# Kernel tuning notes

Hardware: AMD Instinct MI355X
Metric: run time of the kernel (lower is better)

## Reference

```python
import jax, jax.numpy as jnp
import numpy as np

BITS = 4            # OPU.bits
VEC = 64            # OPU.input_vector_len / weight_vector_len
QMAX = 2 ** (BITS - 1) - 1   # 7


def ste_round(x):
    # straight-through round (onn_round)
    return x + jax.lax.stop_gradient(jnp.round(x) - x)


@jax.custom_vjp
def onn_dot_sum(x, w):
    # x: [N, R, VEC], w: [VEC, R, M]
    # per-chunk matmul -> clamp to int8 range -> binarize (>=0 -> 1) -> sum over chunks
    s = jnp.einsum('nrc,crm->nrm', x, w)
    s = jnp.clip(s, -128.0, 127.0)
    return jnp.where(s < 0, 0.0, 1.0).sum(axis=1)  # [N, M]


def _onn_dot_fwd(x, w):
    return onn_dot_sum(x, w), (x, w)


def _onn_dot_bwd(res, g):
    # onn_dot_fun.backward: straight-through past clamp+threshold;
    # each chunk receives the same grad g (sum over chunks).
    x, w = res
    gx = jnp.einsum('nm,crm->nrc', g, w)
    gw = jnp.einsum('nrc,nm->crm', x, g)
    return gx, gw


onn_dot_sum.defvjp(_onn_dot_fwd, _onn_dot_bwd)


def _onn_conv2d(inp, weight):
    B, C, H, W = inp.shape
    Cout, Cin, k, _ = weight.shape
    pad = (k - 1) // 2  # SAME, stride=1
    # im2col (matches torch F.unfold channel-major ordering: C, kh, kw)
    xp = jnp.pad(inp, ((0, 0), (0, 0), (pad, pad), (pad, pad)))
    patches = jnp.stack([xp[:, :, i:i + H, j:j + W]
                         for i in range(k) for j in range(k)], axis=2)  # [B,C,k*k,H,W]
    inp_unf = patches.reshape(B, C * k * k, H * W).transpose(0, 2, 1)    # [B,L,D]
    # weight quantization: STE round + clamp to 4-bit signed range
    scale = (2 ** BITS - 1) / (weight.max() - weight.min() + 1e-9)
    wq = jnp.clip(ste_round(weight * scale), -QMAX, QMAX)
    w_ = wq.reshape(Cout, -1).T                                          # [D, Cout]
    D = C * k * k
    repeats = -(-D // VEC)
    padD = VEC * repeats - D
    x = jnp.pad(inp_unf, ((0, 0), (0, 0), (0, padD))).reshape(B * H * W, repeats, VEC)
    wpad = jnp.pad(w_, ((0, padD), (0, 0)))                              # [VEC*R, Cout]
    wr = wpad.T.reshape(Cout, repeats, VEC).transpose(2, 1, 0)           # [VEC,R,Cout]
    temp = onn_dot_sum(x, wr)                                            # [B*L, Cout]
    return temp.reshape(B, H * W, Cout).transpose(0, 2, 1).reshape(B, Cout, H, W)


def setup_inputs() -> dict:
    key = jax.random.key(0)
    k1, k2 = jax.random.split(key)
    B, Cin, H, W = 16, 128, 32, 32
    Cout, k = 256, 3
    inp = jax.random.normal(k1, (B, Cin, H, W), dtype=jnp.float32)
    fan_in = Cin * k * k
    bound = 1.0 / np.sqrt(fan_in)  # kaiming_uniform with a=sqrt(5)
    weight = jax.random.uniform(k2, (Cout, Cin, k, k), dtype=jnp.float32,
                                minval=-bound, maxval=bound)
    return {"inp": inp, "weight": weight}


def reference(inp, weight):
    return _onn_conv2d(inp, weight)
```

## Files before the change

kernel.cpp:

```cpp
#include <hip/hip_runtime.h>


#define TAU 0.03f
#define HITCAP 2048

typedef short short8 __attribute__((ext_vector_type(8)));
typedef float f32x4 __attribute__((ext_vector_type(4)));
typedef unsigned int uv4 __attribute__((ext_vector_type(4)));

__device__ __forceinline__ unsigned short bf16rn(float v) {
    unsigned u = __float_as_uint(v);
    unsigned r = u + 0x7fffu + ((u >> 16) & 1u);
    return (unsigned short)(r >> 16);
}

__global__ __launch_bounds__(256) void k_prep(const float* __restrict__ w,
                                              const float* __restrict__ inp,
                                              float* __restrict__ pmin,
                                              float* __restrict__ pmax,
                                              unsigned* __restrict__ xpk) {
    if (blockIdx.x < 64) {
        int tid = blockIdx.x * 256 + threadIdx.x;
        float vmin = 1e30f, vmax = -1e30f;
        for (int i = tid; i < 294912; i += 64 * 256) {
            float v = w[i];
            vmin = fminf(vmin, v);
            vmax = fmaxf(vmax, v);
        }
        #pragma unroll
        for (int off = 32; off > 0; off >>= 1) {
            vmin = fminf(vmin, __shfl_down(vmin, off, 64));
            vmax = fmaxf(vmax, __shfl_down(vmax, off, 64));
        }
        __shared__ float smin[4], smax[4];
        int wave = threadIdx.x >> 6;
        if ((threadIdx.x & 63) == 0) { smin[wave] = vmin; smax[wave] = vmax; }
        __syncthreads();
        if (threadIdx.x == 0) {
            #pragma unroll
            for (int i = 1; i < 4; i++) {
                vmin = fminf(vmin, smin[i]);
                vmax = fmaxf(vmax, smax[i]);
            }
            pmin[blockIdx.x] = vmin;
            pmax[blockIdx.x] = vmax;
        }
    } else {
        int bc = blockIdx.x - 64;
        const float* src = inp + (size_t)bc * 1024;
        unsigned* dst = xpk + (size_t)bc * 1156;
        #pragma unroll
        for (int i = 0; i < 5; ++i) {
            int idx = threadIdx.x + i * 256;
            if (idx < 1156) {
                int yy = idx / 34, xx = idx - yy * 34;
                float v = 0.0f;
                int ys = yy - 1, xs_ = xx - 1;
                if ((unsigned)ys < 32u && (unsigned)xs_ < 32u) v = src[ys * 32 + xs_];
                unsigned short h = bf16rn(v);
                float hf = __uint_as_float((unsigned)h << 16);
                unsigned short l = bf16rn(v - hf);
                dst[idx] = (unsigned)h | ((unsigned)l << 16);
            }
        }
    }
}

__device__ __forceinline__ float block_scale(const float* pmin, const float* pmax,
                                             float* sca_lds) {
    int t = threadIdx.x;
    if (t < 64) {
        float vmin = pmin[t];
        float vmax = pmax[t];
        #pragma unroll
        for (int off = 32; off > 0; off >>= 1) {
            vmin = fminf(vmin, __shfl_down(vmin, off, 64));
            vmax = fmaxf(vmax, __shfl_down(vmax, off, 64));
        }
        if (t == 0) {
            float tt = __fadd_rn(__fsub_rn(vmax, vmin), 1e-9f);
            *sca_lds = __fdiv_rn(15.0f, tt);
        }
    }
    __syncthreads();
    return *sca_lds;
}

__global__ __launch_bounds__(256) void k_quantb(const float* __restrict__ w,
                                                const float* __restrict__ pmin,
                                                const float* __restrict__ pmax,
                                                uv4* __restrict__ wqb) {
    __shared__ float sca;
    float s = block_scale(pmin, pmax, &sca);
    int slot = blockIdx.x * 256 + threadIdx.x;
    int lane = slot & 63;
    int sub = slot >> 6;
    int khalf = sub & 1;
    int mt = (sub >> 1) & 3;
    int gr = sub >> 3;
    int g = gr / 18, r = gr - g * 18;
    int m = g * 64 + mt * 16 + (lane & 15);
    int dbase = r * 64 + khalf * 32 + (lane >> 4) * 8;
    const float* wp = w + (size_t)m * 1152 + dbase;
    unsigned o[4];
    #pragma unroll
    for (int p = 0; p < 4; ++p) {
        float q0 = rintf(__fmul_rn(wp[2 * p], s));
        float q1 = rintf(__fmul_rn(wp[2 * p + 1], s));
        q0 = fminf(fmaxf(q0, -7.0f), 7.0f);
        q1 = fminf(fmaxf(q1, -7.0f), 7.0f);
        o[p] = (unsigned)bf16rn(q0) | ((unsigned)bf16rn(q1) << 16);
    }
    uv4 v; v.x = o[0]; v.y = o[1]; v.z = o[2]; v.w = o[3];
    wqb[slot] = v;
}

#define XLD(o) (*reinterpret_cast<const unsigned*>(xwB + (o)))

#define ISSUE_B(rr, dst) do {                                                  \
    const int4* _oa = reinterpret_cast<const int4*>(&ofs_s[(rr) * 64 + quad * 8]); \
    int4 _o0 = _oa[0], _o1 = _oa[1];                                           \
    const int4* _ob = reinterpret_cast<const int4*>(&ofs_s[(rr) * 64 + 32 + quad * 8]); \
    int4 _o2 = _ob[0], _o3 = _ob[1];                                           \
    dst[0] = XLD(_o0.x); dst[1] = XLD(_o0.y); dst[2] = XLD(_o0.z); dst[3] = XLD(_o0.w); \
    dst[4] = XLD(_o1.x); dst[5] = XLD(_o1.y); dst[6] = XLD(_o1.z); dst[7] = XLD(_o1.w); \
    dst[8] = XLD(_o2.x); dst[9] = XLD(_o2.y); dst[10] = XLD(_o2.z); dst[11] = XLD(_o2.w); \
    dst[12] = XLD(_o3.x); dst[13] = XLD(_o3.y); dst[14] = XLD(_o3.z); dst[15] = XLD(_o3.w); \
} while (0)

__global__ __launch_bounds__(256) void k_main(const unsigned* __restrict__ xpk,
                                              const uv4* __restrict__ wqb,
                                              const float* __restrict__ inp,
                                              const float* __restrict__ weight,
                                              const float* __restrict__ pmin,
                                              const float* __restrict__ pmax,
                                              float* __restrict__ out) {
    __shared__ alignas(16) int ofs_s[1152];
    __shared__ unsigned hitbuf[HITCAP];
    __shared__ unsigned hitcnt;
    __shared__ float sca;

    const int t = threadIdx.x;
    if (t == 0) hitcnt = 0u;
    float sc = block_scale(pmin, pmax, &sca);
    for (int k = t; k < 1152; k += 256) {
        int cin = k / 9;
        int rem = k - cin * 9;
        int kh = rem / 3;
        int kw = rem - kh * 3;
        ofs_s[k] = (cin * 1156 + kh * 34 + kw) * 4;
    }
    __syncthreads();

    const int lane = t & 63;
    const int wv = t >> 6;
    const int quad = lane >> 4;
    const int nl = lane & 15;
    const int n0 = blockIdx.x * 64;
    const int g = blockIdx.y;
    const int b = n0 >> 10;

    const int sy_w = ((n0 & 1023) >> 5) + (wv >> 1);
    const int col0 = (wv & 1) * 16;
    const unsigned* __restrict__ xw =
        xpk + (size_t)b * (128 * 1156) + sy_w * 34 + col0 + nl;
    const char* __restrict__ xwB = (const char*)xw;
    const uv4* __restrict__ aw = wqb + (size_t)g * (18 * 512) + lane;

    int counts[4][4] = {};

    unsigned pb[16];
    ISSUE_B(0, pb);
    short8 ac0 = __builtin_bit_cast(short8, aw[0]);
    short8 ac1 = __builtin_bit_cast(short8, aw[64]);

    for (int r = 0; r < 18; ++r) {
        short8 bhi[2], blo[2];
        #pragma unroll
        for (int kh2 = 0; kh2 < 2; ++kh2) {
            union { unsigned d[4]; short8 v; } H, L;
            #pragma unroll
            for (int p = 0; p < 4; ++p) {
                unsigned ua = pb[kh2 * 8 + 2 * p], ub = pb[kh2 * 8 + 2 * p + 1];
                H.d[p] = __builtin_amdgcn_perm(ub, ua, 0x05040100u);
                L.d[p] = __builtin_amdgcn_perm(ub, ua, 0x07060302u);
            }
            bhi[kh2] = H.v;
            blo[kh2] = L.v;
        }

        const int rn = (r < 17) ? r + 1 : 17;
        ISSUE_B(rn, pb);

        f32x4 accs[4];
        unsigned hm = 0u;
        #pragma unroll
        for (int mt = 0; mt < 4; ++mt) {
            const int pn = (mt == 3) ? rn * 512 : (r * 512 + (mt + 1) * 128);
            short8 an0 = __builtin_bit_cast(short8, aw[pn]);
            short8 an1 = __builtin_bit_cast(short8, aw[pn + 64]);

            f32x4 acc = {0.0f, 0.0f, 0.0f, 0.0f};
            acc = __builtin_amdgcn_mfma_f32_16x16x32_bf16(ac0, bhi[0], acc, 0, 0, 0);
            acc = __builtin_amdgcn_mfma_f32_16x16x32_bf16(ac1, bhi[1], acc, 0, 0, 0);
            acc = __builtin_amdgcn_mfma_f32_16x16x32_bf16(ac0, blo[0], acc, 0, 0, 0);
            acc = __builtin_amdgcn_mfma_f32_16x16x32_bf16(ac1, blo[1], acc, 0, 0, 0);
            accs[mt] = acc;
            #pragma unroll
            for (int i = 0; i < 4; ++i) {
                float s = acc[i];
                counts[mt][i] += (s >= 0.0f) ? 1 : 0;
                hm |= (__builtin_fabsf(s) < TAU ? 1u : 0u) << (mt * 4 + i);
            }
            ac0 = an0;
            ac1 = an1;
        }

        if (__any((int)hm)) {
            #pragma unroll
            for (int mt = 0; mt < 4; ++mt)
                #pragma unroll
                for (int i = 0; i < 4; ++i)
                    if (hm & (1u << (mt * 4 + i))) {
                        float s = accs[mt][i];
                        int ge = (s >= 0.0f) ? 1 : 0;
                        unsigned idx = atomicAdd(&hitcnt, 1u);
                        if (idx < (unsigned)HITCAP) {
                            unsigned m = (unsigned)(g * 64 + mt * 16 + quad * 4 + i);
                            unsigned n = (unsigned)(n0 + wv * 16 + nl);
                            hitbuf[idx] = n | ((unsigned)r << 14) | (m << 19)
                                            | ((unsigned)ge << 27);
                        }
                    }
        }
    }

    {
        const int n = n0 + wv * 16 + nl;
        const int p = n & 1023;
        #pragma unroll
        for (int mt = 0; mt < 4; ++mt)
            #pragma unroll
            for (int i = 0; i < 4; ++i) {
                int m = g * 64 + mt * 16 + quad * 4 + i;
                out[(((size_t)(b * 256 + m)) << 10) + p] = (float)counts[mt][i];
            }
    }

    __syncthreads();
    unsigned tot = hitcnt;
    if (tot > (unsigned)HITCAP) tot = (unsigned)HITCAP;
    for (unsigned i = t; i < tot; i += 256) {
        unsigned u = hitbuf[i];
        int n = u & 16383;
        int r = (u >> 14) & 31;
        int m = (u >> 19) & 255;
        int bit = (u >> 27) & 1;
        int bb = n >> 10, p = n & 1023, y = p >> 5, x = p & 31;
        const float* ib = inp + (size_t)bb * (128 * 32 * 32);
        const float* wp = weight + (size_t)m * 1152;
        float s = 0.0f;
        int d = r * 64;
        for (int c = 0; c < 64; ++c, ++d) {
            int ci = d / 9, rem = d - ci * 9;
            int kh = rem / 3, kw = rem - kh * 3;
            int yy = y + kh - 1, xx = x + kw - 1;
            float xv = 0.0f;
            if ((unsigned)yy < 32u && (unsigned)xx < 32u)
                xv = ib[(ci * 32 + yy) * 32 + xx];
            float q = rintf(__fmul_rn(wp[d], sc));
            q = fminf(fmaxf(q, -7.0f), 7.0f);
            s = __fadd_rn(s, __fmul_rn(xv, q));
        }
        int nb = (s >= 0.0f) ? 1 : 0;
        if (nb != bit)
            atomicAdd(&out[(((size_t)(bb * 256 + m)) << 10) + p], nb ? 1.0f : -1.0f);
    }
}

extern "C" void kernel_launch(void* const* d_in, const int* in_sizes, int n_in,
                              void* d_out, int out_size, void* d_ws, size_t ws_size,
                              hipStream_t stream) {
    const float* inp    = (const float*)d_in[0];
    const float* weight = (const float*)d_in[1];
    float* out = (float*)d_out;

    char* ws = (char*)d_ws;
    float*    pmin  = (float*)(ws + 0);
    float*    pmax  = (float*)(ws + 256);
    uv4*      wqb   = (uv4*)(ws + 1024);
    unsigned* xpk   = (unsigned*)(ws + 590848);

    k_prep<<<2112, 256, 0, stream>>>(weight, inp, pmin, pmax, xpk);
    k_quantb<<<144, 256, 0, stream>>>(weight, pmin, pmax, wqb);

    dim3 grid(256, 4);
    k_main<<<grid, 256, 0, stream>>>(xpk, wqb, inp, weight, pmin, pmax, out);
}
```

Baseline: 127.8 us.

## Double output-channel tile per block to reuse gathered activations across 128 channels

Each block now computes 128 output channels instead of 64, halving the grid's y dimension so each gathered im2col activation fragment feeds eight MFMA tiles instead of four. The sign counting switches to a negative-count via the float sign bit, and near-threshold detection uses a wave ballot accumulated into a 64-bit mask. Activation addressing uses a 32-bit byte offset from the base pointer. The cost is more accumulator and count registers per thread and fewer blocks, which can lower occupancy.

```diff
diff --git a/kernel.cpp b/kernel.cpp
--- a/kernel.cpp
+++ b/kernel.cpp
@@ -115,7 +115,7 @@
     wqb[slot] = v;
 }
 
-#define XLD(o) (*reinterpret_cast<const unsigned*>(xwB + (o)))
+#define XLD(o) (*reinterpret_cast<const unsigned*>(xpkB + (xdelta + (unsigned)(o))))
 
 #define ISSUE_B(rr, dst) do {                                                  \
     const int4* _oa = reinterpret_cast<const int4*>(&ofs_s[(rr) * 64 + quad * 8]); \
@@ -127,6 +127,8 @@
     dst[8] = XLD(_o2.x); dst[9] = XLD(_o2.y); dst[10] = XLD(_o2.z); dst[11] = XLD(_o2.w); \
     dst[12] = XLD(_o3.x); dst[13] = XLD(_o3.y); dst[14] = XLD(_o3.z); dst[15] = XLD(_o3.w); \
 } while (0)
+
+#define AIDX(rr, mm) ((((mm) >> 2) * 9216) + (rr) * 512 + (((mm) & 3) * 128))
 
 __global__ __launch_bounds__(256) void k_main(const unsigned* __restrict__ xpk,
                                               const uv4* __restrict__ wqb,
@@ -162,12 +164,13 @@
 
     const int sy_w = ((n0 & 1023) >> 5) + (wv >> 1);
     const int col0 = (wv & 1) * 16;
-    const unsigned* __restrict__ xw =
-        xpk + (size_t)b * (128 * 1156) + sy_w * 34 + col0 + nl;
-    const char* __restrict__ xwB = (const char*)xw;
-    const uv4* __restrict__ aw = wqb + (size_t)g * (18 * 512) + lane;
-
-    int counts[4][4] = {};
+    const char* __restrict__ xpkB = (const char*)xpk;
+    const unsigned xdelta =
+        ((unsigned)b * (128u * 1156u) + (unsigned)(sy_w * 34 + col0 + nl)) * 4u;
+    const uv4* __restrict__ aw = wqb + (size_t)g * (2 * 18 * 512) + lane;
+
+    unsigned negcnt[8][4] = {};
+    unsigned long long hitacc = 0ull;
 
     unsigned pb[16];
     ISSUE_B(0, pb);
@@ -192,11 +195,10 @@
         const int rn = (r < 17) ? r + 1 : 17;
         ISSUE_B(rn, pb);
 
-        f32x4 accs[4];
-        unsigned hm = 0u;
-        #pragma unroll
-        for (int mt = 0; mt < 4; ++mt) {
-            const int pn = (mt == 3) ? rn * 512 : (r * 512 + (mt + 1) * 128);
+        f32x4 accs[8];
+        #pragma unroll
+        for (int mt = 0; mt < 8; ++mt) {
+            const int pn = (mt == 7) ? AIDX(rn, 0) : AIDX(r, mt + 1);
             short8 an0 = __builtin_bit_cast(short8, aw[pn]);
             short8 an1 = __builtin_bit_cast(short8, aw[pn + 64]);
 
@@ -208,30 +210,31 @@
             accs[mt] = acc;
             #pragma unroll
             for (int i = 0; i < 4; ++i) {
-                float s = acc[i];
-                counts[mt][i] += (s >= 0.0f) ? 1 : 0;
-                hm |= (__builtin_fabsf(s) < TAU ? 1u : 0u) << (mt * 4 + i);
+                negcnt[mt][i] += __float_as_uint(acc[i]) >> 31;
+                hitacc |= __ballot(__builtin_fabsf(acc[i]) < TAU);
             }
             ac0 = an0;
             ac1 = an1;
         }
 
-        if (__any((int)hm)) {
-            #pragma unroll
-            for (int mt = 0; mt < 4; ++mt)
+        if (hitacc) {
+            #pragma unroll
+            for (int mt = 0; mt < 8; ++mt)
                 #pragma unroll
-                for (int i = 0; i < 4; ++i)
-                    if (hm & (1u << (mt * 4 + i))) {
-                        float s = accs[mt][i];
-                        int ge = (s >= 0.0f) ? 1 : 0;
+                for (int i = 0; i < 4; ++i) {
+                    float s = accs[mt][i];
+                    if (__builtin_fabsf(s) < TAU) {
+                        unsigned ge = (__float_as_uint(s) >> 31) ^ 1u;
                         unsigned idx = atomicAdd(&hitcnt, 1u);
                         if (idx < (unsigned)HITCAP) {
-                            unsigned m = (unsigned)(g * 64 + mt * 16 + quad * 4 + i);
+                            unsigned m = (unsigned)(g * 128 + mt * 16 + quad * 4 + i);
                             unsigned n = (unsigned)(n0 + wv * 16 + nl);
                             hitbuf[idx] = n | ((unsigned)r << 14) | (m << 19)
-                                            | ((unsigned)ge << 27);
+                                            | (ge << 27);
                         }
                     }
+                }
+            hitacc = 0ull;
         }
     }
 
@@ -239,11 +242,12 @@
         const int n = n0 + wv * 16 + nl;
         const int p = n & 1023;
         #pragma unroll
-        for (int mt = 0; mt < 4; ++mt)
+        for (int mt = 0; mt < 8; ++mt)
             #pragma unroll
             for (int i = 0; i < 4; ++i) {
-                int m = g * 64 + mt * 16 + quad * 4 + i;
-                out[(((size_t)(b * 256 + m)) << 10) + p] = (float)counts[mt][i];
+                int m = g * 128 + mt * 16 + quad * 4 + i;
+                out[(((size_t)(b * 256 + m)) << 10) + p] =
+                    (float)(18u - negcnt[mt][i]);
             }
     }
 
@@ -294,6 +298,6 @@
     k_prep<<<2112, 256, 0, stream>>>(weight, inp, pmin, pmax, xpk);
     k_quantb<<<144, 256, 0, stream>>>(weight, pmin, pmax, wqb);
 
-    dim3 grid(256, 4);
+    dim3 grid(256, 2);
     k_main<<<grid, 256, 0, stream>>>(xpk, wqb, inp, weight, pmin, pmax, out);
 }
```

Measured after the change: 124.2 us. 1.03x faster.
